# Performance work log

Hardware: AMD Instinct MI355X
Metric: run time of the kernel (lower is better)

Reference implementation:

```python
import jax, jax.numpy as jnp
import numpy as np

K = 1024  # num_embeddings
D = 256   # embedding_dim
COMMIT = 0.25

def setup_inputs() -> dict:
    key = jax.random.key(0)
    k1, k2 = jax.random.split(key)
    z = jax.random.normal(k1, (32, 256, 32, 32), dtype=jnp.float32)
    # matches nn.Embedding init uniform_(-1/K, 1/K)
    emb = jax.random.uniform(k2, (K, D), dtype=jnp.float32, minval=-1.0 / K, maxval=1.0 / K)
    return {"z": z, "emb": emb}

def reference(z, emb):
    B, C, H, W = z.shape
    zp = jnp.transpose(z, (0, 2, 3, 1))            # (B,H,W,C)
    z_flat = zp.reshape(-1, C)                      # (N,D)
    # squared euclidean distances (N,K)
    d = (jnp.sum(z_flat * z_flat, axis=1, keepdims=True)
         + jnp.sum(emb * emb, axis=1)
         - 2.0 * z_flat @ emb.T)
    idx = jnp.argmin(d, axis=1)                     # (N,)
    quantized_flat = emb[idx]                       # gather == one-hot @ emb
    quantized = quantized_flat.reshape(zp.shape)    # (B,H,W,C)
    e_latent_loss = jnp.mean((jax.lax.stop_gradient(quantized) - zp) ** 2)
    q_latent_loss = jnp.mean((quantized - jax.lax.stop_gradient(zp)) ** 2)
    loss = q_latent_loss + COMMIT * e_latent_loss
    # straight-through estimator
    quantized_st = zp + jax.lax.stop_gradient(quantized - zp)
    # perplexity: avg one-hot probs == normalized counts
    N = z_flat.shape[0]
    counts = jnp.zeros((K,), dtype=jnp.float32).at[idx].add(1.0)
    avg_probs = counts / N
    perplexity = jnp.exp(-jnp.sum(avg_probs * jnp.log(avg_probs + 1e-10)))
    out = jnp.transpose(quantized_st, (0, 3, 1, 2))  # (B,C,H,W)
    return (out, loss, perplexity)
```

## Files before the change

kernel.cpp:

```cpp
#include <hip/hip_runtime.h>
#include <math.h>

#define KC 1024
#define DD 256
#define NROWS 32768
#define NELEM 8388608

typedef _Float16 f16;
typedef __attribute__((ext_vector_type(8))) _Float16 f16x8;
typedef __attribute__((ext_vector_type(16))) float f32x16;

#define KEY_SCALE 2097152.0f
#define KEY_INV   (1.0f / 2097152.0f)

__global__ void vq_prep_kernel(const float* __restrict__ emb, f16* __restrict__ emb_h,
                               float* __restrict__ c_sq) {
    const int tid = threadIdx.x;
    const int gt = blockIdx.x * 256 + tid;
    {
        int k = blockIdx.x * 4 + (tid >> 6);
        int lane = tid & 63;
        float4 v = *(const float4*)(emb + (size_t)k * DD + lane * 4);
        float s = v.x * v.x + v.y * v.y + v.z * v.z + v.w * v.w;
        #pragma unroll
        for (int off = 32; off > 0; off >>= 1) s += __shfl_down(s, off);
        if (lane == 0) c_sq[k] = s;
    }
    if (gt < 32768) {
        int code = gt & 1023;
        int kg = gt >> 10;
        const float* p = emb + (size_t)code * DD + kg * 8;
        float4 v0 = *(const float4*)p;
        float4 v1 = *(const float4*)(p + 4);
        f16x8 hcv;
        hcv[0] = (f16)v0.x; hcv[1] = (f16)v0.y; hcv[2] = (f16)v0.z; hcv[3] = (f16)v0.w;
        hcv[4] = (f16)v1.x; hcv[5] = (f16)v1.y; hcv[6] = (f16)v1.z; hcv[7] = (f16)v1.w;
        *(f16x8*)(emb_h + (size_t)gt * 8) = hcv;
    }
}

__global__ __launch_bounds__(512, 4)
void vq_argmin_kernel(const float* __restrict__ z, const f16* __restrict__ emb_h,
                      const float* __restrict__ c_sq, int* __restrict__ idx_g,
                      float* __restrict__ loss_blk) {
    __shared__ __align__(16) f16 z_s[32 * 64 * 8];
    __shared__ int   bl_key[8][64];
    __shared__ float zsq_part[8][64];

    const int tid = threadIdx.x;
    const int n0 = blockIdx.x * 64;
    const int b = n0 >> 10;
    const int hw0 = n0 & 1023;

    {
        const int r = tid & 63;
        const int kq = tid >> 6;
        const float* zp = z + (size_t)b * (DD * 1024) + hw0 + r;
        float sq = 0.f;
        #pragma unroll
        for (int it = 0; it < 4; ++it) {
            int kg = kq * 4 + it;
            f16x8 hv;
            #pragma unroll
            for (int j = 0; j < 8; ++j) {
                float v = zp[(size_t)(kg * 8 + j) * 1024];
                sq += v * v;
                hv[j] = (f16)v;
            }
            *(f16x8*)&z_s[(kg * 64 + r) * 8] = hv;
        }
        zsq_part[kq][r] = sq;
    }
    __syncthreads();

    const int m = tid & 31;
    const int h = (tid >> 5) & 1;
    const int w = tid >> 6;

    int kmin0 = 0x7FFFFFFF;
    int kmin1 = 0x7FFFFFFF;

    for (int c = 0; c < 4; ++c) {
        const int cb = w * 128 + c * 32;
        const f16* ebp = emb_h + (size_t)h * 8192 + (size_t)(cb + m) * 8;

        f32x16 acc0, acc1;
        #pragma unroll
        for (int i = 0; i < 16; ++i) { acc0[i] = 0.f; acc1[i] = 0.f; }

        #pragma unroll 2
        for (int ks = 0; ks < 16; ++ks) {
            const f16* za = z_s + ((size_t)(2 * ks + h) * 64 + m) * 8;
            f16x8 zb0 = *(const f16x8*)(za);
            f16x8 zb1 = *(const f16x8*)(za + 256);
            f16x8 ea  = *(const f16x8*)(ebp + (size_t)ks * 16384);
            acc0 = __builtin_amdgcn_mfma_f32_32x32x16_f16(ea, zb0, acc0, 0, 0, 0);
            acc1 = __builtin_amdgcn_mfma_f32_32x32x16_f16(ea, zb1, acc1, 0, 0, 0);
        }

        #pragma unroll
        for (int reg = 0; reg < 16; ++reg) {
            int code = cb + (reg & 3) + 8 * (reg >> 2) + 4 * h;
            float cs = c_sq[code];
            float s0 = fmaf(-2.f, acc0[reg], cs);
            float s1 = fmaf(-2.f, acc1[reg], cs);
            kmin0 = min(kmin0, (int)(s0 * KEY_SCALE) * 1024 + code);
            kmin1 = min(kmin1, (int)(s1 * KEY_SCALE) * 1024 + code);
        }
    }

    kmin0 = min(kmin0, __shfl_xor(kmin0, 32));
    kmin1 = min(kmin1, __shfl_xor(kmin1, 32));
    if (h == 0) { bl_key[w][m] = kmin0; bl_key[w][32 + m] = kmin1; }
    __syncthreads();

    if (tid < 64) {
        int k = bl_key[0][tid];
        #pragma unroll
        for (int w2 = 1; w2 < 8; ++w2) k = min(k, bl_key[w2][tid]);
        idx_g[n0 + tid] = k & 1023;
        float zq = 0.f;
        #pragma unroll
        for (int p = 0; p < 8; ++p) zq += zsq_part[p][tid];
        float lr = (float)(k >> 10) * KEY_INV + zq;
        #pragma unroll
        for (int off = 32; off > 0; off >>= 1) lr += __shfl_down(lr, off);
        if (tid == 0) loss_blk[blockIdx.x] = lr;
    }
}

__global__ __launch_bounds__(512, 4)
void vq_out_kernel(const float* __restrict__ emb, const int* __restrict__ idx_g,
                   const float* __restrict__ loss_blk, float* __restrict__ out,
                   float* __restrict__ out_tail) {
    __shared__ float Qt[128][65];
    __shared__ int   idx_s[64];

    const int tid = threadIdx.x;

    if (blockIdx.x == 1024) {
        __shared__ int   hist[KC];
        __shared__ float wsum[8];
        for (int k = tid; k < KC; k += 512) hist[k] = 0;
        __syncthreads();
        for (int i = tid; i < NROWS; i += 512)
            atomicAdd(&hist[idx_g[i]], 1);
        __syncthreads();
        float s = 0.f;
        for (int k = tid; k < KC; k += 512) {
            float pr = (float)hist[k] * (1.0f / (float)NROWS);
            s += pr * logf(pr + 1e-10f);
        }
        float lv = (tid < 512) ? loss_blk[tid] : 0.f;
        s = s;
        #pragma unroll
        for (int off = 32; off > 0; off >>= 1) {
            s  += __shfl_down(s, off);
            lv += __shfl_down(lv, off);
        }
        if ((tid & 63) == 0) { wsum[tid >> 6] = s; Qt[0][tid >> 6] = lv; }
        __syncthreads();
        if (tid == 0) {
            float ent = 0.f, loss_tot = 0.f;
            #pragma unroll
            for (int p = 0; p < 8; ++p) { ent += wsum[p]; loss_tot += Qt[0][p]; }
            out_tail[0] = 1.25f * loss_tot * (1.0f / (float)NELEM);
            out_tail[1] = expf(-ent);
        }
        return;
    }

    const int tile = blockIdx.x >> 1;
    const int ch0 = (blockIdx.x & 1) * 128;
    const int n0 = tile * 64;
    const int b = n0 >> 10;
    const int hw0 = n0 & 1023;

    if (tid < 64) idx_s[tid] = idx_g[n0 + tid];
    __syncthreads();

    {
        int r = tid & 63;
        int p = tid >> 6;
        const float* ep = emb + (size_t)idx_s[r] * DD + ch0 + p * 16;
        float4 v0 = *(const float4*)(ep);
        float4 v1 = *(const float4*)(ep + 4);
        float4 v2 = *(const float4*)(ep + 8);
        float4 v3 = *(const float4*)(ep + 12);
        float vv[16] = {v0.x, v0.y, v0.z, v0.w, v1.x, v1.y, v1.z, v1.w,
                        v2.x, v2.y, v2.z, v2.w, v3.x, v3.y, v3.z, v3.w};
        #pragma unroll
        for (int g = 0; g < 16; ++g)
            Qt[p * 16 + g][r] = vv[g];
    }
    __syncthreads();

    {
        int lane = tid & 63;
        int w = tid >> 6;
        const size_t base = (size_t)b * (DD * 1024) + hw0 + lane;
        #pragma unroll
        for (int g = 0; g < 16; ++g) {
            int ch = w * 16 + g;
            out[base + (size_t)(ch0 + ch) * 1024] = Qt[ch][lane];
        }
    }
}

extern "C" void kernel_launch(void* const* d_in, const int* in_sizes, int n_in,
                              void* d_out, int out_size, void* d_ws, size_t ws_size,
                              hipStream_t stream) {
    const float* z = (const float*)d_in[0];
    const float* emb = (const float*)d_in[1];
    float* out = (float*)d_out;

    char* wsb = (char*)d_ws;
    f16* emb_h = (f16*)wsb;
    float* c_sq = (float*)(wsb + 524288);
    int* idx_g = (int*)(wsb + 528384);
    float* loss_blk = (float*)(wsb + 659456);

    hipLaunchKernelGGL(vq_prep_kernel, dim3(256), dim3(256), 0, stream,
                       emb, emb_h, c_sq);
    hipLaunchKernelGGL(vq_argmin_kernel, dim3(512), dim3(512), 0, stream,
                       z, emb_h, c_sq, idx_g, loss_blk);
    hipLaunchKernelGGL(vq_out_kernel, dim3(1025), dim3(512), 0, stream,
                       emb, idx_g, loss_blk, out, out + NELEM);
}
```

Baseline: 126.0 us.

## Split codebook across two blocks per tile and merge argmin via atomicMin

The argmin kernel now launches twice as many blocks, each scanning half of the codebook for a 64-row tile, and combines the per-row packed distance/index keys with global atomicMin into a workspace that the prep kernel initialises. The loss reduction moves into the tail block of the output kernel, which reads the packed keys and per-row z norms. Launch bounds rise to 8 blocks per SM to increase occupancy. In exchange, each tile's z data is loaded and converted twice, global atomics are added, and tighter launch bounds may force register spills.

```diff
diff --git a/kernel.cpp b/kernel.cpp
--- a/kernel.cpp
+++ b/kernel.cpp
@@ -14,9 +14,10 @@
 #define KEY_INV   (1.0f / 2097152.0f)
 
 __global__ void vq_prep_kernel(const float* __restrict__ emb, f16* __restrict__ emb_h,
-                               float* __restrict__ c_sq) {
+                               float* __restrict__ c_sq, int* __restrict__ key_ws) {
     const int tid = threadIdx.x;
     const int gt = blockIdx.x * 256 + tid;
+    if (gt < 32768) key_ws[gt] = 0x7FFFFFFF;
     {
         int k = blockIdx.x * 4 + (tid >> 6);
         int lane = tid & 63;
@@ -39,16 +40,19 @@
     }
 }
 
-__global__ __launch_bounds__(512, 4)
+__global__ __launch_bounds__(512, 8)
 void vq_argmin_kernel(const float* __restrict__ z, const f16* __restrict__ emb_h,
-                      const float* __restrict__ c_sq, int* __restrict__ idx_g,
-                      float* __restrict__ loss_blk) {
+                      const float* __restrict__ c_sq, float* __restrict__ zsq_g,
+                      int* __restrict__ key_ws) {
     __shared__ __align__(16) f16 z_s[32 * 64 * 8];
     __shared__ int   bl_key[8][64];
     __shared__ float zsq_part[8][64];
 
     const int tid = threadIdx.x;
-    const int n0 = blockIdx.x * 64;
+    const int bid = blockIdx.x;
+    const int tile = bid & 511;
+    const int cg = bid >> 9;
+    const int n0 = tile * 64;
     const int b = n0 >> 10;
     const int hw0 = n0 & 1023;
 
@@ -80,8 +84,8 @@
     int kmin0 = 0x7FFFFFFF;
     int kmin1 = 0x7FFFFFFF;
 
-    for (int c = 0; c < 4; ++c) {
-        const int cb = w * 128 + c * 32;
+    for (int c = 0; c < 2; ++c) {
+        const int cb = cg * 512 + w * 64 + c * 32;
         const f16* ebp = emb_h + (size_t)h * 8192 + (size_t)(cb + m) * 8;
 
         f32x16 acc0, acc1;
@@ -118,20 +122,19 @@
         int k = bl_key[0][tid];
         #pragma unroll
         for (int w2 = 1; w2 < 8; ++w2) k = min(k, bl_key[w2][tid]);
-        idx_g[n0 + tid] = k & 1023;
-        float zq = 0.f;
-        #pragma unroll
-        for (int p = 0; p < 8; ++p) zq += zsq_part[p][tid];
-        float lr = (float)(k >> 10) * KEY_INV + zq;
-        #pragma unroll
-        for (int off = 32; off > 0; off >>= 1) lr += __shfl_down(lr, off);
-        if (tid == 0) loss_blk[blockIdx.x] = lr;
+        atomicMin(&key_ws[n0 + tid], k);
+        if (cg == 0) {
+            float zq = 0.f;
+            #pragma unroll
+            for (int p = 0; p < 8; ++p) zq += zsq_part[p][tid];
+            zsq_g[n0 + tid] = zq;
+        }
     }
 }
 
 __global__ __launch_bounds__(512, 4)
-void vq_out_kernel(const float* __restrict__ emb, const int* __restrict__ idx_g,
-                   const float* __restrict__ loss_blk, float* __restrict__ out,
+void vq_out_kernel(const float* __restrict__ emb, const int* __restrict__ key_ws,
+                   const float* __restrict__ zsq_g, float* __restrict__ out,
                    float* __restrict__ out_tail) {
     __shared__ float Qt[128][65];
     __shared__ int   idx_s[64];
@@ -143,16 +146,18 @@
         __shared__ float wsum[8];
         for (int k = tid; k < KC; k += 512) hist[k] = 0;
         __syncthreads();
-        for (int i = tid; i < NROWS; i += 512)
-            atomicAdd(&hist[idx_g[i]], 1);
+        float lv = 0.f;
+        for (int i = tid; i < NROWS; i += 512) {
+            int k = key_ws[i];
+            atomicAdd(&hist[k & 1023], 1);
+            lv += (float)(k >> 10) * KEY_INV + zsq_g[i];
+        }
         __syncthreads();
         float s = 0.f;
         for (int k = tid; k < KC; k += 512) {
             float pr = (float)hist[k] * (1.0f / (float)NROWS);
             s += pr * logf(pr + 1e-10f);
         }
-        float lv = (tid < 512) ? loss_blk[tid] : 0.f;
-        s = s;
         #pragma unroll
         for (int off = 32; off > 0; off >>= 1) {
             s  += __shfl_down(s, off);
@@ -176,7 +181,7 @@
     const int b = n0 >> 10;
     const int hw0 = n0 & 1023;
 
-    if (tid < 64) idx_s[tid] = idx_g[n0 + tid];
+    if (tid < 64) idx_s[tid] = key_ws[n0 + tid] & 1023;
     __syncthreads();
 
     {
@@ -217,13 +222,13 @@
     char* wsb = (char*)d_ws;
     f16* emb_h = (f16*)wsb;
     float* c_sq = (float*)(wsb + 524288);
-    int* idx_g = (int*)(wsb + 528384);
-    float* loss_blk = (float*)(wsb + 659456);
+    int* key_ws = (int*)(wsb + 528384);
+    float* zsq_g = (float*)(wsb + 659456);
 
     hipLaunchKernelGGL(vq_prep_kernel, dim3(256), dim3(256), 0, stream,
-                       emb, emb_h, c_sq);
-    hipLaunchKernelGGL(vq_argmin_kernel, dim3(512), dim3(512), 0, stream,
-                       z, emb_h, c_sq, idx_g, loss_blk);
+                       emb, emb_h, c_sq, key_ws);
+    hipLaunchKernelGGL(vq_argmin_kernel, dim3(1024), dim3(512), 0, stream,
+                       z, emb_h, c_sq, zsq_g, key_ws);
     hipLaunchKernelGGL(vq_out_kernel, dim3(1025), dim3(512), 0, stream,
-                       emb, idx_g, loss_blk, out, out + NELEM);
-}
+                       emb, key_ws, zsq_g, out, out + NELEM);
+}
```

After: 143.9 us. +14.3%, slower.
